# Kernel optimization log

Hardware: AMD Instinct MI355X
Metric: run time of the kernel (lower is better)

## Reference

```python
import jax, jax.numpy as jnp
import numpy as np

L, NFEAT, J, S = 100000, 256, 128, 8  # nodes, features, hidden, samples_per_k


def setup_inputs() -> dict:
    key = jax.random.key(0)
    ks = jax.random.split(key, 8)
    X = jax.random.normal(ks[0], (L, NFEAT), dtype=jnp.float32)
    # sampled 2-permutation neighbor indices (first and second element of each permutation)
    idx0 = jax.random.randint(ks[1], (S, L), 0, L)
    idx1 = jax.random.randint(ks[2], (S, L), 0, L)
    def lin(k, fan_in, fan_out):
        bound = 1.0 / np.sqrt(fan_in)
        kw, kb = jax.random.split(k)
        W = jax.random.uniform(kw, (fan_in, fan_out), jnp.float32, -bound, bound)
        b = jax.random.uniform(kb, (fan_out,), jnp.float32, -bound, bound)
        return W, b
    W_h1, b_h1 = lin(ks[3], NFEAT, J)      # h1: Linear(nfeat, J)
    W_g1, b_g1 = lin(ks[4], 2 * J, J)      # g1: Linear(2J, J)
    W_f, b_f = lin(ks[5], J, 2)            # final1: Linear(J, 2)
    return {"X": X, "W_h1": W_h1, "b_h1": b_h1, "W_g1": W_g1, "b_g1": b_g1,
            "W_f": W_f, "b_f": b_f, "idx0": idx0, "idx1": idx1}


def reference(X, W_h1, b_h1, W_g1, b_g1, W_f, b_f, idx0, idx1):
    # h(x) = relu(h1(x)); since h is only ever applied to rows of X, compute once and gather.
    H = jax.nn.relu(X @ W_h1 + b_h1)                     # (L, J)
    # fk(k=2): mean over samples of g(cat(h(X[perm0]), h(X[perm1])))
    pair = jnp.concatenate([H[idx0], H[idx1]], axis=-1)  # (S, L, 2J) irregular gather
    E = jnp.mean(jax.nn.relu(pair @ W_g1 + b_g1), axis=0)  # (L, J)
    E = jax.nn.relu(E)                                   # relu of mean of relus (faithful)
    # E = g(cat(h(X), E))
    E = jax.nn.relu(jnp.concatenate([H, E], axis=-1) @ W_g1 + b_g1)  # (L, J)
    # yhat = final1(E)
    return E @ W_f + b_f                                 # (L, 2)
```

## Files before the change

### kernel.cpp

```cpp
#include <hip/hip_runtime.h>

#define L_NODES 100000
#define NFEAT   256
#define JDIM    128

typedef __bf16 bf16x8 __attribute__((ext_vector_type(8)));
typedef __bf16 bf16x4 __attribute__((ext_vector_type(4)));
typedef float  floatx4 __attribute__((ext_vector_type(4)));

__global__ __launch_bounds__(256) void k_prep(
    const float* __restrict__ Wh, const float* __restrict__ Wg,
    __bf16* __restrict__ WtH, __bf16* __restrict__ WtG2)
{
    int i = blockIdx.x * 256 + threadIdx.x;
    int n = i >> 8, k = i & 255;
    WtH[i] = (__bf16)Wh[k * JDIM + n];
    int n2 = i >> 7, k2 = i & 127;
    WtG2[i] = (n2 < 128) ? (__bf16)Wg[k2 * JDIM + n2]
                         : (__bf16)Wg[(128 + k2) * JDIM + (n2 - 128)];
}

__global__ __launch_bounds__(256, 3) void k_h1uv(
    const float* __restrict__ X, const __bf16* __restrict__ WtH,
    const __bf16* __restrict__ WtG2, const float* __restrict__ b,
    __bf16* __restrict__ U, __bf16* __restrict__ V)
{
    __shared__ __bf16 Sm[64 * 264];
    __shared__ __bf16 Hs[64 * 136];

    const int tid  = threadIdx.x;
    const int row0 = blockIdx.x * 64;
    const int wave = tid >> 6, lane = tid & 63;
    const int lm = lane & 15, lq = lane >> 4;

    floatx4 xa[16];
    #pragma unroll
    for (int it = 0; it < 16; ++it) {
        int f4  = it * 256 + tid;
        int row = f4 >> 6, c4 = f4 & 63;
        int grow = row0 + row; if (grow >= L_NODES) grow = L_NODES - 1;
        xa[it] = __builtin_nontemporal_load(
                     reinterpret_cast<const floatx4*>(X + (size_t)grow * NFEAT + c4 * 4));
    }
    #pragma unroll
    for (int it = 0; it < 16; ++it) {
        int f4  = it * 256 + tid;
        int row = f4 >> 6, c4 = f4 & 63;
        bf16x4 o;
        o[0]=(__bf16)xa[it][0]; o[1]=(__bf16)xa[it][1];
        o[2]=(__bf16)xa[it][2]; o[3]=(__bf16)xa[it][3];
        *(bf16x4*)&Sm[row * 264 + c4 * 4] = o;
    }

    bf16x8 b1[2][8];
    #pragma unroll
    for (int nt = 0; nt < 2; ++nt) {
        int ntg = wave * 2 + nt;
        #pragma unroll
        for (int ks = 0; ks < 8; ++ks)
            b1[nt][ks] = *(const bf16x8*)(WtH + (size_t)(ntg * 16 + lm) * 256 + ks * 32 + lq * 8);
    }
    __syncthreads();

    floatx4 acc1[4][2] = {};
    #pragma unroll
    for (int ks = 0; ks < 8; ++ks) {
        bf16x8 af[4];
        #pragma unroll
        for (int t = 0; t < 4; ++t)
            af[t] = *(const bf16x8*)&Sm[(t * 16 + lm) * 264 + ks * 32 + lq * 8];
        #pragma unroll
        for (int t = 0; t < 4; ++t)
            #pragma unroll
            for (int nt = 0; nt < 2; ++nt)
                acc1[t][nt] = __builtin_amdgcn_mfma_f32_16x16x32_bf16(
                    af[t], b1[nt][ks], acc1[t][nt], 0, 0, 0);
    }

    #pragma unroll
    for (int nt = 0; nt < 2; ++nt) {
        int col = (wave * 2 + nt) * 16 + lm;
        float bias = b[col];
        #pragma unroll
        for (int t = 0; t < 4; ++t)
            #pragma unroll
            for (int p = 0; p < 4; ++p)
                Hs[(t * 16 + lq * 4 + p) * 136 + col] =
                    (__bf16)fmaxf(acc1[t][nt][p] + bias, 0.f);
    }
    __syncthreads();

    #pragma unroll
    for (int h = 0; h < 2; ++h) {
        bf16x8 b2h[2][4];
        #pragma unroll
        for (int nt = 0; nt < 2; ++nt) {
            int ntg = wave * 4 + h * 2 + nt;
            #pragma unroll
            for (int ks = 0; ks < 4; ++ks)
                b2h[nt][ks] = *(const bf16x8*)(WtG2 + (size_t)(ntg * 16 + lm) * 128 + ks * 32 + lq * 8);
        }
        floatx4 acc2[4][2] = {};
        #pragma unroll
        for (int ks = 0; ks < 4; ++ks) {
            bf16x8 af[4];
            #pragma unroll
            for (int t = 0; t < 4; ++t)
                af[t] = *(const bf16x8*)&Hs[(t * 16 + lm) * 136 + ks * 32 + lq * 8];
            #pragma unroll
            for (int t = 0; t < 4; ++t)
                #pragma unroll
                for (int nt = 0; nt < 2; ++nt)
                    acc2[t][nt] = __builtin_amdgcn_mfma_f32_16x16x32_bf16(
                        af[t], b2h[nt][ks], acc2[t][nt], 0, 0, 0);
        }
        #pragma unroll
        for (int nt = 0; nt < 2; ++nt) {
            int col = (wave * 4 + h * 2 + nt) * 16 + lm;
            #pragma unroll
            for (int t = 0; t < 4; ++t)
                #pragma unroll
                for (int p = 0; p < 4; ++p)
                    Sm[(t * 16 + lq * 4 + p) * 264 + col] = (__bf16)acc2[t][nt][p];
        }
    }
    __syncthreads();

    #pragma unroll
    for (int it = 0; it < 8; ++it) {
        int fid = it * 256 + tid;
        int row = fid >> 5, c8 = fid & 31;
        int grow = row0 + row;
        if (grow < L_NODES) {
            int col = c8 * 8;
            bf16x8 v = *(bf16x8*)&Sm[row * 264 + col];
            if (col < 128) *(bf16x8*)(U + (size_t)grow * JDIM + col) = v;
            else           *(bf16x8*)(V + (size_t)grow * JDIM + (col - 128)) = v;
        }
    }
}

__global__ __launch_bounds__(256, 4) void k_gfinal(
    const __bf16* __restrict__ U, const __bf16* __restrict__ V,
    const __bf16* __restrict__ WtGv, const float* __restrict__ bg,
    const float* __restrict__ Wf, const float* __restrict__ bf,
    const int* __restrict__ idx0, const int* __restrict__ idx1,
    float* __restrict__ out)
{
    __shared__ int    sidx[2][8][64];
    __shared__ __bf16 E1s[64 * 136];
    __shared__ __bf16 Us [64 * 136];
    float (*part)[64][2] = (float (*)[64][2])&sidx[0][0][0];

    const int tid  = threadIdx.x;
    const int row0 = blockIdx.x * 64;
    const int wave = tid >> 6, lane = tid & 63;
    const int lm = lane & 15, lq = lane >> 4;

    #pragma unroll
    for (int it = 0; it < 4; ++it) {
        int fid = it * 256 + tid;
        int m = fid >> 9, rem = fid & 511;
        int s = rem >> 6, il = rem & 63;
        int gr = row0 + il; if (gr >= L_NODES) gr = L_NODES - 1;
        const int* ip = (m ? idx1 : idx0) + (size_t)s * L_NODES + gr;
        sidx[m][s][il] = __builtin_nontemporal_load(ip);
    }
    #pragma unroll
    for (int it = 0; it < 4; ++it) {
        int fid = it * 256 + tid;
        int r = fid >> 4, c8 = fid & 15;
        int g = row0 + r; if (g >= L_NODES) g = L_NODES - 1;
        *(bf16x8*)&Us[r * 136 + c8 * 8] = *(const bf16x8*)(U + (size_t)g * JDIM + c8 * 8);
    }
    __syncthreads();

    {
        const int c0 = (tid & 15) * 8;
        const int rb = tid >> 4;
        float bias[8];
        *(float4*)&bias[0] = *(const float4*)(bg + c0);
        *(float4*)&bias[4] = *(const float4*)(bg + c0 + 4);

        float acc[4][8] = {};
        bf16x8 uA[4], vA[4], uB[4], vB[4];

        auto LOADP = [&](int s, bf16x8 (&uu)[4], bf16x8 (&vv)[4]) {
            #pragma unroll
            for (int rr = 0; rr < 4; ++rr) {
                int r = rb + rr * 16;
                int a0 = sidx[0][s][r], a1 = sidx[1][s][r];
                uu[rr] = *(const bf16x8*)(U + (size_t)a0 * JDIM + c0);
                vv[rr] = *(const bf16x8*)(V + (size_t)a1 * JDIM + c0);
            }
        };
        auto ACCUM = [&](bf16x8 (&uu)[4], bf16x8 (&vv)[4]) {
            #pragma unroll
            for (int rr = 0; rr < 4; ++rr)
                #pragma unroll
                for (int p = 0; p < 8; ++p)
                    acc[rr][p] += fmaxf((float)uu[rr][p] + (float)vv[rr][p] + bias[p], 0.f);
        };

        LOADP(0, uA, vA);
        #pragma unroll
        for (int s = 0; s < 8; ++s) {
            if ((s & 1) == 0) {
                if (s < 7) LOADP(s + 1, uB, vB);
                ACCUM(uA, vA);
            } else {
                if (s < 7) LOADP(s + 1, uA, vA);
                ACCUM(uB, vB);
            }
        }

        #pragma unroll
        for (int rr = 0; rr < 4; ++rr) {
            int r = rb + rr * 16;
            bf16x8 o;
            #pragma unroll
            for (int p = 0; p < 8; ++p)
                o[p] = (__bf16)fmaxf(acc[rr][p] * 0.125f, 0.f);
            *(bf16x8*)&E1s[r * 136 + c0] = o;
        }
    }
    __syncthreads();

    bf16x8 b3[2][4];
    #pragma unroll
    for (int nt = 0; nt < 2; ++nt) {
        int ntg = wave * 2 + nt;
        #pragma unroll
        for (int ks = 0; ks < 4; ++ks)
            b3[nt][ks] = *(const bf16x8*)(WtGv + (size_t)(ntg * 16 + lm) * 128 + ks * 32 + lq * 8);
    }

    floatx4 acc[4][2] = {};
    #pragma unroll
    for (int ks = 0; ks < 4; ++ks) {
        bf16x8 af[4];
        #pragma unroll
        for (int t = 0; t < 4; ++t)
            af[t] = *(const bf16x8*)&E1s[(t * 16 + lm) * 136 + ks * 32 + lq * 8];
        #pragma unroll
        for (int t = 0; t < 4; ++t)
            #pragma unroll
            for (int nt = 0; nt < 2; ++nt)
                acc[t][nt] = __builtin_amdgcn_mfma_f32_16x16x32_bf16(
                    af[t], b3[nt][ks], acc[t][nt], 0, 0, 0);
    }

    float bias[2], wf0[2], wf1[2];
    #pragma unroll
    for (int nt = 0; nt < 2; ++nt) {
        int col = (wave * 2 + nt) * 16 + lm;
        bias[nt] = bg[col];
        wf0[nt] = Wf[col * 2 + 0];
        wf1[nt] = Wf[col * 2 + 1];
    }
    #pragma unroll
    for (int t = 0; t < 4; ++t) {
        float p0[4], p1[4];
        #pragma unroll
        for (int p = 0; p < 4; ++p) {
            int r = t * 16 + lq * 4 + p;
            float a0 = 0.f, a1 = 0.f;
            #pragma unroll
            for (int nt = 0; nt < 2; ++nt) {
                int col = (wave * 2 + nt) * 16 + lm;
                float e2 = fmaxf((float)Us[r * 136 + col] + acc[t][nt][p] + bias[nt], 0.f);
                a0 = fmaf(e2, wf0[nt], a0);
                a1 = fmaf(e2, wf1[nt], a1);
            }
            p0[p] = a0; p1[p] = a1;
        }
        #pragma unroll
        for (int m = 1; m <= 8; m <<= 1)
            #pragma unroll
            for (int p = 0; p < 4; ++p) {
                p0[p] += __shfl_xor(p0[p], m, 16);
                p1[p] += __shfl_xor(p1[p], m, 16);
            }
        if (lm == 0)
            #pragma unroll
            for (int p = 0; p < 4; ++p) {
                part[wave][t * 16 + lq * 4 + p][0] = p0[p];
                part[wave][t * 16 + lq * 4 + p][1] = p1[p];
            }
    }
    __syncthreads();

    if (tid < 128) {
        int row = tid >> 1, o = tid & 1;
        int grow = row0 + row;
        if (grow < L_NODES) {
            float v = part[0][row][o] + part[1][row][o] + part[2][row][o]
                    + part[3][row][o] + bf[o];
            __builtin_nontemporal_store(v, &out[(size_t)grow * 2 + o]);
        }
    }
}

extern "C" void kernel_launch(void* const* d_in, const int* in_sizes, int n_in,
                              void* d_out, int out_size, void* d_ws, size_t ws_size,
                              hipStream_t stream) {
    const float* X    = (const float*)d_in[0];
    const float* W_h1 = (const float*)d_in[1];
    const float* b_h1 = (const float*)d_in[2];
    const float* W_g1 = (const float*)d_in[3];
    const float* b_g1 = (const float*)d_in[4];
    const float* W_f  = (const float*)d_in[5];
    const float* b_f  = (const float*)d_in[6];
    const int*   idx0 = (const int*)d_in[7];
    const int*   idx1 = (const int*)d_in[8];
    float* out = (float*)d_out;

    __bf16* U    = (__bf16*)d_ws;
    __bf16* V    = U   + (size_t)L_NODES * JDIM;
    __bf16* WtH  = V   + (size_t)L_NODES * JDIM;
    __bf16* WtG2 = WtH + 32768;
    __bf16* WtGv = WtG2 + 128 * 128;

    k_prep<<<128, 256, 0, stream>>>(W_h1, W_g1, WtH, WtG2);
    k_h1uv<<<(L_NODES + 63) / 64, 256, 0, stream>>>(X, WtH, WtG2, b_h1, U, V);
    k_gfinal<<<(L_NODES + 63) / 64, 256, 0, stream>>>(U, V, WtGv, b_g1, W_f, b_f,
                                                      idx0, idx1, out);
}
```

Baseline: 249.7 us.

## Double k_h1uv row tile to 128 and alias H buffer into shared Sm

The h1/UV kernel now processes 128 rows per block instead of 64. Each wave reuses its register-resident weight fragments over twice as many rows, and the number of blocks is halved. The separate Hs shared buffer is dropped: H is written into Sm after an extra barrier, and both halves of the second GEMM are kept in registers before being written back. In exchange the kernel needs far more registers (32 X vectors, 64 accumulators), occupancy drops to 2 blocks per SIMD group, and there are fewer blocks to spread across the CUs.

```diff
diff --git a/kernel.cpp b/kernel.cpp
--- a/kernel.cpp
+++ b/kernel.cpp
@@ -20,22 +20,21 @@
                          : (__bf16)Wg[(128 + k2) * JDIM + (n2 - 128)];
 }
 
-__global__ __launch_bounds__(256, 3) void k_h1uv(
+__global__ __launch_bounds__(256, 2) void k_h1uv(
     const float* __restrict__ X, const __bf16* __restrict__ WtH,
     const __bf16* __restrict__ WtG2, const float* __restrict__ b,
     __bf16* __restrict__ U, __bf16* __restrict__ V)
 {
-    __shared__ __bf16 Sm[64 * 264];
-    __shared__ __bf16 Hs[64 * 136];
+    __shared__ __bf16 Sm[128 * 264];
 
     const int tid  = threadIdx.x;
-    const int row0 = blockIdx.x * 64;
+    const int row0 = blockIdx.x * 128;
     const int wave = tid >> 6, lane = tid & 63;
     const int lm = lane & 15, lq = lane >> 4;
 
-    floatx4 xa[16];
-    #pragma unroll
-    for (int it = 0; it < 16; ++it) {
+    floatx4 xa[32];
+    #pragma unroll
+    for (int it = 0; it < 32; ++it) {
         int f4  = it * 256 + tid;
         int row = f4 >> 6, c4 = f4 & 63;
         int grow = row0 + row; if (grow >= L_NODES) grow = L_NODES - 1;
@@ -43,7 +42,7 @@
                      reinterpret_cast<const floatx4*>(X + (size_t)grow * NFEAT + c4 * 4));
     }
     #pragma unroll
-    for (int it = 0; it < 16; ++it) {
+    for (int it = 0; it < 32; ++it) {
         int f4  = it * 256 + tid;
         int row = f4 >> 6, c4 = f4 & 63;
         bf16x4 o;
@@ -62,72 +61,100 @@
     }
     __syncthreads();
 
-    floatx4 acc1[4][2] = {};
+    floatx4 acc1[8][2] = {};
     #pragma unroll
     for (int ks = 0; ks < 8; ++ks) {
-        bf16x8 af[4];
-        #pragma unroll
-        for (int t = 0; t < 4; ++t)
+        bf16x8 af[8];
+        #pragma unroll
+        for (int t = 0; t < 8; ++t)
             af[t] = *(const bf16x8*)&Sm[(t * 16 + lm) * 264 + ks * 32 + lq * 8];
         #pragma unroll
-        for (int t = 0; t < 4; ++t)
+        for (int t = 0; t < 8; ++t)
             #pragma unroll
             for (int nt = 0; nt < 2; ++nt)
                 acc1[t][nt] = __builtin_amdgcn_mfma_f32_16x16x32_bf16(
                     af[t], b1[nt][ks], acc1[t][nt], 0, 0, 0);
     }
+    __syncthreads();
 
     #pragma unroll
     for (int nt = 0; nt < 2; ++nt) {
         int col = (wave * 2 + nt) * 16 + lm;
         float bias = b[col];
         #pragma unroll
-        for (int t = 0; t < 4; ++t)
+        for (int t = 0; t < 8; ++t)
             #pragma unroll
             for (int p = 0; p < 4; ++p)
-                Hs[(t * 16 + lq * 4 + p) * 136 + col] =
+                Sm[(t * 16 + lq * 4 + p) * 136 + col] =
                     (__bf16)fmaxf(acc1[t][nt][p] + bias, 0.f);
     }
     __syncthreads();
 
-    #pragma unroll
-    for (int h = 0; h < 2; ++h) {
+    floatx4 acc2a[8][2] = {}, acc2b[8][2] = {};
+    {
         bf16x8 b2h[2][4];
         #pragma unroll
         for (int nt = 0; nt < 2; ++nt) {
-            int ntg = wave * 4 + h * 2 + nt;
+            int ntg = wave * 4 + nt;
             #pragma unroll
             for (int ks = 0; ks < 4; ++ks)
                 b2h[nt][ks] = *(const bf16x8*)(WtG2 + (size_t)(ntg * 16 + lm) * 128 + ks * 32 + lq * 8);
         }
-        floatx4 acc2[4][2] = {};
         #pragma unroll
         for (int ks = 0; ks < 4; ++ks) {
-            bf16x8 af[4];
-            #pragma unroll
-            for (int t = 0; t < 4; ++t)
-                af[t] = *(const bf16x8*)&Hs[(t * 16 + lm) * 136 + ks * 32 + lq * 8];
-            #pragma unroll
-            for (int t = 0; t < 4; ++t)
+            bf16x8 af[8];
+            #pragma unroll
+            for (int t = 0; t < 8; ++t)
+                af[t] = *(const bf16x8*)&Sm[(t * 16 + lm) * 136 + ks * 32 + lq * 8];
+            #pragma unroll
+            for (int t = 0; t < 8; ++t)
                 #pragma unroll
                 for (int nt = 0; nt < 2; ++nt)
-                    acc2[t][nt] = __builtin_amdgcn_mfma_f32_16x16x32_bf16(
-                        af[t], b2h[nt][ks], acc2[t][nt], 0, 0, 0);
-        }
+                    acc2a[t][nt] = __builtin_amdgcn_mfma_f32_16x16x32_bf16(
+                        af[t], b2h[nt][ks], acc2a[t][nt], 0, 0, 0);
+        }
+    }
+    {
+        bf16x8 b2h[2][4];
+        #pragma unroll
+        for (int nt = 0; nt < 2; ++nt) {
+            int ntg = wave * 4 + 2 + nt;
+            #pragma unroll
+            for (int ks = 0; ks < 4; ++ks)
+                b2h[nt][ks] = *(const bf16x8*)(WtG2 + (size_t)(ntg * 16 + lm) * 128 + ks * 32 + lq * 8);
+        }
+        #pragma unroll
+        for (int ks = 0; ks < 4; ++ks) {
+            bf16x8 af[8];
+            #pragma unroll
+            for (int t = 0; t < 8; ++t)
+                af[t] = *(const bf16x8*)&Sm[(t * 16 + lm) * 136 + ks * 32 + lq * 8];
+            #pragma unroll
+            for (int t = 0; t < 8; ++t)
+                #pragma unroll
+                for (int nt = 0; nt < 2; ++nt)
+                    acc2b[t][nt] = __builtin_amdgcn_mfma_f32_16x16x32_bf16(
+                        af[t], b2h[nt][ks], acc2b[t][nt], 0, 0, 0);
+        }
+    }
+    __syncthreads();
+
+    #pragma unroll
+    for (int h = 0; h < 2; ++h)
         #pragma unroll
         for (int nt = 0; nt < 2; ++nt) {
             int col = (wave * 4 + h * 2 + nt) * 16 + lm;
             #pragma unroll
-            for (int t = 0; t < 4; ++t)
+            for (int t = 0; t < 8; ++t)
                 #pragma unroll
                 for (int p = 0; p < 4; ++p)
-                    Sm[(t * 16 + lq * 4 + p) * 264 + col] = (__bf16)acc2[t][nt][p];
-        }
-    }
-    __syncthreads();
-
-    #pragma unroll
-    for (int it = 0; it < 8; ++it) {
+                    Sm[(t * 16 + lq * 4 + p) * 264 + col] =
+                        (__bf16)(h ? acc2b[t][nt][p] : acc2a[t][nt][p]);
+        }
+    __syncthreads();
+
+    #pragma unroll
+    for (int it = 0; it < 16; ++it) {
         int fid = it * 256 + tid;
         int row = fid >> 5, c8 = fid & 31;
         int grow = row0 + row;
@@ -322,7 +349,7 @@
     __bf16* WtGv = WtG2 + 128 * 128;
 
     k_prep<<<128, 256, 0, stream>>>(W_h1, W_g1, WtH, WtG2);
-    k_h1uv<<<(L_NODES + 63) / 64, 256, 0, stream>>>(X, WtH, WtG2, b_h1, U, V);
+    k_h1uv<<<(L_NODES + 127) / 128, 256, 0, stream>>>(X, WtH, WtG2, b_h1, U, V);
     k_gfinal<<<(L_NODES + 63) / 64, 256, 0, stream>>>(U, V, WtGv, b_g1, W_f, b_f,
                                                       idx0, idx1, out);
 }
```

After: 249.0 us. No clear change (-0.3%).
